# Kernel tuning notes

Measured on AMD Instinct MI355X. Metric: run time of the kernel, lower is better.

The kernel has to match this reference:

```python
import jax, jax.numpy as jnp
import numpy as np

PROCESSING_STEPS = 3


def setup_inputs() -> dict:
    key = jax.random.key(0)
    ks = jax.random.split(key, 6)
    N, D, G = 500000, 128, 4096
    x = jax.random.normal(ks[0], (N, D), dtype=jnp.float32)
    # torch LSTM param layout: [4*hidden, input] and [4*hidden, hidden], gates i,f,g,o
    s = 1.0 / np.sqrt(D)
    W_ih = jax.random.uniform(ks[1], (4 * D, 2 * D), minval=-s, maxval=s, dtype=jnp.float32)
    W_hh = jax.random.uniform(ks[2], (4 * D, D), minval=-s, maxval=s, dtype=jnp.float32)
    b_ih = jax.random.uniform(ks[3], (4 * D,), minval=-s, maxval=s, dtype=jnp.float32)
    b_hh = jax.random.uniform(ks[4], (4 * D,), minval=-s, maxval=s, dtype=jnp.float32)
    index = jnp.sort(jax.random.randint(ks[5], (N,), 0, G, dtype=jnp.int64))
    return {"x": x, "W_ih": W_ih, "W_hh": W_hh, "b_ih": b_ih, "b_hh": b_hh,
            "index": index, "dim_size": G}


def _lstm_cell(inp, h, c, W_ih, W_hh, b_ih, b_hh):
    gates = inp @ W_ih.T + h @ W_hh.T + (b_ih + b_hh)  # [G, 4D]
    i, f, g, o = jnp.split(gates, 4, axis=-1)
    c = jax.nn.sigmoid(f) * c + jax.nn.sigmoid(i) * jnp.tanh(g)
    h = jax.nn.sigmoid(o) * jnp.tanh(c)
    return h, c


def reference(x, W_ih, W_hh, b_ih, b_hh, index, dim_size):
    N, D = x.shape
    h = jnp.zeros((dim_size, D), dtype=x.dtype)
    c = jnp.zeros((dim_size, D), dtype=x.dtype)
    q_star = jnp.zeros((dim_size, 2 * D), dtype=x.dtype)
    for _ in range(PROCESSING_STEPS):
        h, c = _lstm_cell(q_star, h, c, W_ih, W_hh, b_ih, b_hh)
        q = h  # [G, D]
        e = jnp.sum(x * q[index], axis=-1)  # [N]
        # segment softmax (numerically stable)
        m = jax.ops.segment_max(e, index, num_segments=dim_size)
        m = jnp.where(jnp.isfinite(m), m, 0.0)  # guard empty segments
        ex = jnp.exp(e - m[index])
        s = jax.ops.segment_sum(ex, index, num_segments=dim_size)
        a = ex / jnp.maximum(s, 1e-16)[index]  # [N]
        r = jax.ops.segment_sum(a[:, None] * x, index, num_segments=dim_size)  # [G, D]
        q_star = jnp.concatenate([q, r], axis=-1)
    return q_star
```

## Files before the change

### kernel.cpp

```cpp
#include <hip/hip_runtime.h>
#include <math.h>

#define D 128

__device__ __forceinline__ float sigmoidf_(float x) { return 1.f / (1.f + __expf(-x)); }

__global__ void prep_kernel(const float* __restrict__ W_ih, const float* __restrict__ W_hh,
                            const float* __restrict__ b_ih, const float* __restrict__ b_hh,
                            const int* __restrict__ idx, int N, int G,
                            float* __restrict__ Wc, int* __restrict__ seg_off,
                            float* __restrict__ b_sum, float* __restrict__ h1,
                            float* __restrict__ c1) {
    int b = blockIdx.x, t = threadIdx.x;
    if (b < 256) {
        int i = b * 256 + t;
        int j = i >> 7, k = i & (D - 1);
        Wc[i] = W_ih[(size_t)j * (2 * D) + k] + W_hh[i];
    } else if (b < 273) {
        int g = (b - 256) * 256 + t;
        if (g <= G) {
            int lo = 0, hi = N;
            while (lo < hi) {
                int mid = (lo + hi) >> 1;
                if (idx[mid] < g) lo = mid + 1; else hi = mid;
            }
            seg_off[g] = lo;
        }
    } else {
        for (int i = t; i < 4 * D; i += 256) b_sum[i] = b_ih[i] + b_hh[i];
        if (t < D) {
            float bi = b_ih[t] + b_hh[t];
            float bg = b_ih[2 * D + t] + b_hh[2 * D + t];
            float bo = b_ih[3 * D + t] + b_hh[3 * D + t];
            float c = sigmoidf_(bi) * tanhf(bg);
            c1[t] = c;
            h1[t] = sigmoidf_(bo) * tanhf(c);
        }
    }
}

__global__ __launch_bounds__(256) void attn_kernel(
    const float* __restrict__ x, const int* __restrict__ seg_off,
    const float* __restrict__ q, int q_stride,
    float* __restrict__ r_out, int r_stride, int G) {
    int g = blockIdx.x;
    if (g >= G) return;
    int tid = threadIdx.x;
    int wave = tid >> 6, lane = tid & 63;
    int half = lane >> 5, col4 = lane & 31;

    __shared__ float sm[4], ss[4];
    __shared__ float sacc[4][D];

    int start = seg_off[g], end = seg_off[g + 1];
    int count = end - start;
    int chunk = (count + 3) >> 2;
    int wsr = start + wave * chunk;
    int wer = min(wsr + chunk, end);

    const float4* x4 = (const float4*)x;
    const float4* q4 = (const float4*)(q + (size_t)g * q_stride);
    float4 qv = q4[col4];

    float m = -INFINITY, s = 0.f;
    float4 acc = {0.f, 0.f, 0.f, 0.f};

    if (wsr < wer) {
        int last = wer - 1;
        int ngroups = (wer - wsr + 7) >> 3;
        for (int it = 0; it < ngroups; ++it) {
            int base = wsr + it * 8;
            int ra = min(base + 0 + half, last);
            int rb = min(base + 2 + half, last);
            int rc = min(base + 4 + half, last);
            int rd = min(base + 6 + half, last);
            float4 xa = x4[(size_t)ra * 32 + col4];
            float4 xb = x4[(size_t)rb * 32 + col4];
            float4 xc = x4[(size_t)rc * 32 + col4];
            float4 xd = x4[(size_t)rd * 32 + col4];

            float pa = xa.x * qv.x + xa.y * qv.y + xa.z * qv.z + xa.w * qv.w;
            float pb = xb.x * qv.x + xb.y * qv.y + xb.z * qv.z + xb.w * qv.w;
            float pc = xc.x * qv.x + xc.y * qv.y + xc.z * qv.z + xc.w * qv.w;
            float pd = xd.x * qv.x + xd.y * qv.y + xd.z * qv.z + xd.w * qv.w;
#pragma unroll
            for (int off = 1; off < 32; off <<= 1) {
                pa += __shfl_xor(pa, off);
                pb += __shfl_xor(pb, off);
                pc += __shfl_xor(pc, off);
                pd += __shfl_xor(pd, off);
            }
            float oa = __shfl_xor(pa, 32);
            float ob = __shfl_xor(pb, 32);
            float oc = __shfl_xor(pc, 32);
            float od = __shfl_xor(pd, 32);
            float pae = half ? oa : pa, pao = half ? pa : oa;
            float pbe = half ? ob : pb, pbo = half ? pb : ob;
            float pce = half ? oc : pc, pco = half ? pc : oc;
            float pde = half ? od : pd, pdo = half ? pd : od;
            pae = (base + 0 < wer) ? pae : -INFINITY;
            pao = (base + 1 < wer) ? pao : -INFINITY;
            pbe = (base + 2 < wer) ? pbe : -INFINITY;
            pbo = (base + 3 < wer) ? pbo : -INFINITY;
            pce = (base + 4 < wer) ? pce : -INFINITY;
            pco = (base + 5 < wer) ? pco : -INFINITY;
            pde = (base + 6 < wer) ? pde : -INFINITY;
            pdo = (base + 7 < wer) ? pdo : -INFINITY;

            float mn = fmaxf(fmaxf(fmaxf(pae, pao), fmaxf(pbe, pbo)),
                             fmaxf(fmaxf(pce, pco), fmaxf(pde, pdo)));
            mn = fmaxf(m, mn);
            float al = __expf(m - mn);
            float wae = __expf(pae - mn), wao = __expf(pao - mn);
            float wbe = __expf(pbe - mn), wbo = __expf(pbo - mn);
            float wce = __expf(pce - mn), wco = __expf(pco - mn);
            float wde = __expf(pde - mn), wdo = __expf(pdo - mn);
            float sg = (wae + wao) + (wbe + wbo) + ((wce + wco) + (wde + wdo));
            s = s * al + sg;
            float wsa = half ? wao : wae;
            float wsb = half ? wbo : wbe;
            float wsc = half ? wco : wce;
            float wsd = half ? wdo : wde;
            float tx = wsa * xa.x + wsb * xb.x + wsc * xc.x + wsd * xd.x;
            float ty = wsa * xa.y + wsb * xb.y + wsc * xc.y + wsd * xd.y;
            float tz = wsa * xa.z + wsb * xb.z + wsc * xc.z + wsd * xd.z;
            float tw = wsa * xa.w + wsb * xb.w + wsc * xc.w + wsd * xd.w;
            acc.x = acc.x * al + tx;
            acc.y = acc.y * al + ty;
            acc.z = acc.z * al + tz;
            acc.w = acc.w * al + tw;
            m = mn;
        }
    }
    acc.x += __shfl_xor(acc.x, 32);
    acc.y += __shfl_xor(acc.y, 32);
    acc.z += __shfl_xor(acc.z, 32);
    acc.w += __shfl_xor(acc.w, 32);

    if (lane == 0) { sm[wave] = m; ss[wave] = s; }
    if (half == 0) *(float4*)&sacc[wave][col4 * 4] = acc;
    __syncthreads();

    if (tid < D) {
        float m0 = sm[0], m1 = sm[1], m2 = sm[2], m3 = sm[3];
        float mstar = fmaxf(fmaxf(m0, m1), fmaxf(m2, m3));
        float r = 0.f;
        if (mstar > -INFINITY) {
            float e0 = __expf(m0 - mstar), e1 = __expf(m1 - mstar);
            float e2 = __expf(m2 - mstar), e3 = __expf(m3 - mstar);
            float stot = ss[0] * e0 + ss[1] * e1 + ss[2] * e2 + ss[3] * e3;
            float at = sacc[0][tid] * e0 + sacc[1][tid] * e1
                     + sacc[2][tid] * e2 + sacc[3][tid] * e3;
            r = at / fmaxf(stot, 1e-16f);
        }
        r_out[(size_t)g * r_stride + tid] = r;
    }
}

__global__ __launch_bounds__(256) void gates_gemm_kernel(
    const float* __restrict__ A1, int sA1,
    const float* __restrict__ W1,
    const float* __restrict__ A2,
    const float* __restrict__ W2, int sW2,
    const float* __restrict__ bias,
    float* __restrict__ gates) {
    __shared__ float As[32][72];
    __shared__ float Ws[32][72];
    int t = threadIdx.x;
    int tx = t & 15, ty = t >> 4;
    int g0 = blockIdx.x * 64, j0 = blockIdx.y * 64;
    int lr = t & 63;
    int lk = (t >> 6) * 8;

    float acc[4][4];
#pragma unroll
    for (int i = 0; i < 4; ++i)
#pragma unroll
        for (int j = 0; j < 4; ++j) acc[i][j] = 0.f;

    for (int phase = 0; phase < 2; ++phase) {
        const float* A = phase ? A2 : A1;
        int sA = phase ? D : sA1;
        const float* W = phase ? W2 : W1;
        int sW = phase ? sW2 : D;
        for (int kk = 0; kk < D; kk += 32) {
            float4 a0 = *(const float4*)&A[(size_t)(g0 + lr) * sA + kk + lk];
            float4 a1 = *(const float4*)&A[(size_t)(g0 + lr) * sA + kk + lk + 4];
            float4 w0 = *(const float4*)&W[(size_t)(j0 + lr) * sW + kk + lk];
            float4 w1 = *(const float4*)&W[(size_t)(j0 + lr) * sW + kk + lk + 4];
            __syncthreads();
            As[lk + 0][lr] = a0.x; As[lk + 1][lr] = a0.y; As[lk + 2][lr] = a0.z; As[lk + 3][lr] = a0.w;
            As[lk + 4][lr] = a1.x; As[lk + 5][lr] = a1.y; As[lk + 6][lr] = a1.z; As[lk + 7][lr] = a1.w;
            Ws[lk + 0][lr] = w0.x; Ws[lk + 1][lr] = w0.y; Ws[lk + 2][lr] = w0.z; Ws[lk + 3][lr] = w0.w;
            Ws[lk + 4][lr] = w1.x; Ws[lk + 5][lr] = w1.y; Ws[lk + 6][lr] = w1.z; Ws[lk + 7][lr] = w1.w;
            __syncthreads();
#pragma unroll
            for (int k = 0; k < 32; ++k) {
                float4 av = *(const float4*)&As[k][ty * 4];
                float4 bv = *(const float4*)&Ws[k][tx * 4];
                float aa[4] = {av.x, av.y, av.z, av.w};
                float bb[4] = {bv.x, bv.y, bv.z, bv.w};
#pragma unroll
                for (int i = 0; i < 4; ++i)
#pragma unroll
                    for (int j = 0; j < 4; ++j)
                        acc[i][j] = fmaf(aa[i], bb[j], acc[i][j]);
            }
        }
    }
#pragma unroll
    for (int i = 0; i < 4; ++i) {
        size_t row = (size_t)(g0 + ty * 4 + i);
        int jb = j0 + tx * 4;
        float4 o;
        o.x = acc[i][0] + bias[jb + 0];
        o.y = acc[i][1] + bias[jb + 1];
        o.z = acc[i][2] + bias[jb + 2];
        o.w = acc[i][3] + bias[jb + 3];
        *(float4*)&gates[row * 512 + jb] = o;
    }
}

__global__ void cell_kernel(const float* __restrict__ gates,
                            const float* __restrict__ c_prev, int c_stride,
                            float* __restrict__ c_out,
                            float* __restrict__ h_out, int h_stride,
                            int total) {
    int t = blockIdx.x * blockDim.x + threadIdx.x;
    if (t >= total) return;
    int g = t >> 7, k = t & (D - 1);
    const float* grow = gates + (size_t)g * 512;
    float ig = grow[k];
    float fg = grow[D + k];
    float gg = grow[2 * D + k];
    float og = grow[3 * D + k];
    float cp = c_prev[(size_t)g * c_stride + k];
    float c = sigmoidf_(fg) * cp + sigmoidf_(ig) * tanhf(gg);
    float h = sigmoidf_(og) * tanhf(c);
    c_out[t] = c;
    h_out[(size_t)g * h_stride + k] = h;
}

extern "C" void kernel_launch(void* const* d_in, const int* in_sizes, int n_in,
                              void* d_out, int out_size, void* d_ws, size_t ws_size,
                              hipStream_t stream) {
    const float* x      = (const float*)d_in[0];
    const float* W_ih   = (const float*)d_in[1];
    const float* W_hh   = (const float*)d_in[2];
    const float* b_ih   = (const float*)d_in[3];
    const float* b_hh   = (const float*)d_in[4];
    const int*   index  = (const int*)d_in[5];
    int N = in_sizes[5];
    int G = out_size / (2 * D);
    float* out = (float*)d_out;

    float* ws = (float*)d_ws;
    float* Wc     = ws;
    float* b_sum  = Wc + 4 * D * D;
    float* h1     = b_sum + 4 * D;
    float* c1     = h1 + D;
    float* r1     = c1 + D;
    float* h2     = r1 + (size_t)G * D;
    float* c2     = h2 + (size_t)G * D;
    float* r2     = c2 + (size_t)G * D;
    float* gatesb = r2 + (size_t)G * D;
    int* seg_off  = (int*)(gatesb + (size_t)G * 4 * D);
    float* c3     = r1;

    prep_kernel<<<274, 256, 0, stream>>>(W_ih, W_hh, b_ih, b_hh, index, N, G,
                                         Wc, seg_off, b_sum, h1, c1);

    attn_kernel<<<G, 256, 0, stream>>>(x, seg_off, h1, 0, r1, D, G);

    gates_gemm_kernel<<<dim3(G / 64, 8), 256, 0, stream>>>(
        h1, 0, Wc, r1, W_ih + D, 2 * D, b_sum, gatesb);
    cell_kernel<<<(G * D + 255) / 256, 256, 0, stream>>>(gatesb, c1, 0, c2, h2, D, G * D);
    attn_kernel<<<G, 256, 0, stream>>>(x, seg_off, h2, D, r2, D, G);

    gates_gemm_kernel<<<dim3(G / 64, 8), 256, 0, stream>>>(
        h2, D, Wc, r2, W_ih + D, 2 * D, b_sum, gatesb);
    cell_kernel<<<(G * D + 255) / 256, 256, 0, stream>>>(gatesb, c2, D, c3, out, 2 * D, G * D);
    attn_kernel<<<G, 256, 0, stream>>>(x, seg_off, out, 2 * D, out + D, 2 * D, G);
}
```

Baseline: 494.6 us.

## Double-buffer segment rows through LDS with register-staged prefetch in attention kernel

The attention kernel now walks each segment in tiles of 32 rows. The whole block cooperatively loads each tile into a double-buffered 32 KB shared-memory array, prefetching the next tile into registers while the current one is processed. This replaces the old scheme, where each wave owned a contiguous quarter of the segment and read rows straight from global memory. The goal is to overlap global loads with compute and to keep coalesced, fully occupied loads. In exchange it adds a __syncthreads per tile, uses 32 KB of LDS per block (which lowers occupancy), and does more masked work at tile tails.

```diff
diff --git a/kernel.cpp b/kernel.cpp
--- a/kernel.cpp
+++ b/kernel.cpp
@@ -42,21 +42,20 @@
 __global__ __launch_bounds__(256) void attn_kernel(
     const float* __restrict__ x, const int* __restrict__ seg_off,
     const float* __restrict__ q, int q_stride,
-    float* __restrict__ r_out, int r_stride, int G) {
+    float* __restrict__ r_out, int r_stride, int G, int N) {
     int g = blockIdx.x;
     if (g >= G) return;
     int tid = threadIdx.x;
     int wave = tid >> 6, lane = tid & 63;
     int half = lane >> 5, col4 = lane & 31;
 
+    __shared__ float xs[2][32 * D];
     __shared__ float sm[4], ss[4];
     __shared__ float sacc[4][D];
 
     int start = seg_off[g], end = seg_off[g + 1];
     int count = end - start;
-    int chunk = (count + 3) >> 2;
-    int wsr = start + wave * chunk;
-    int wer = min(wsr + chunk, end);
+    int T = (count + 31) >> 5;
 
     const float4* x4 = (const float4*)x;
     const float4* q4 = (const float4*)(q + (size_t)g * q_stride);
@@ -65,19 +64,45 @@
     float m = -INFINITY, s = 0.f;
     float4 acc = {0.f, 0.f, 0.f, 0.f};
 
-    if (wsr < wer) {
-        int last = wer - 1;
-        int ngroups = (wer - wsr + 7) >> 3;
-        for (int it = 0; it < ngroups; ++it) {
-            int base = wsr + it * 8;
-            int ra = min(base + 0 + half, last);
-            int rb = min(base + 2 + half, last);
-            int rc = min(base + 4 + half, last);
-            int rd = min(base + 6 + half, last);
-            float4 xa = x4[(size_t)ra * 32 + col4];
-            float4 xb = x4[(size_t)rb * 32 + col4];
-            float4 xc = x4[(size_t)rc * 32 + col4];
-            float4 xd = x4[(size_t)rd * 32 + col4];
+    size_t gmax = (size_t)N * 32 - 1;
+
+    if (T > 0) {
+        size_t b4 = (size_t)start * 32;
+        size_t i0 = b4 + tid, i1 = b4 + 256 + tid, i2 = b4 + 512 + tid, i3 = b4 + 768 + tid;
+        float4 v0 = x4[i0 < gmax ? i0 : gmax];
+        float4 v1 = x4[i1 < gmax ? i1 : gmax];
+        float4 v2 = x4[i2 < gmax ? i2 : gmax];
+        float4 v3 = x4[i3 < gmax ? i3 : gmax];
+        *(float4*)&xs[0][(tid) * 4]       = v0;
+        *(float4*)&xs[0][(256 + tid) * 4] = v1;
+        *(float4*)&xs[0][(512 + tid) * 4] = v2;
+        *(float4*)&xs[0][(768 + tid) * 4] = v3;
+    }
+
+    for (int t = 0; t < T; ++t) {
+        int cur = t & 1;
+        __syncthreads();
+
+        float4 st0, st1, st2, st3;
+        bool more = (t + 1 < T);
+        if (more) {
+            size_t b4 = (size_t)(start + (t + 1) * 32) * 32;
+            size_t i0 = b4 + tid, i1 = b4 + 256 + tid, i2 = b4 + 512 + tid, i3 = b4 + 768 + tid;
+            st0 = x4[i0 < gmax ? i0 : gmax];
+            st1 = x4[i1 < gmax ? i1 : gmax];
+            st2 = x4[i2 < gmax ? i2 : gmax];
+            st3 = x4[i3 < gmax ? i3 : gmax];
+        }
+
+        int tbase = t * 32 + wave * 8;
+        if (tbase < count) {
+            int vr = count - tbase;
+            const float* ls = &xs[cur][0];
+            int rb = wave * 8 + half;
+            float4 xa = *(const float4*)&ls[(rb + 0) * D + col4 * 4];
+            float4 xb = *(const float4*)&ls[(rb + 2) * D + col4 * 4];
+            float4 xc = *(const float4*)&ls[(rb + 4) * D + col4 * 4];
+            float4 xd = *(const float4*)&ls[(rb + 6) * D + col4 * 4];
 
             float pa = xa.x * qv.x + xa.y * qv.y + xa.z * qv.z + xa.w * qv.w;
             float pb = xb.x * qv.x + xb.y * qv.y + xb.z * qv.z + xb.w * qv.w;
@@ -98,14 +123,13 @@
             float pbe = half ? ob : pb, pbo = half ? pb : ob;
             float pce = half ? oc : pc, pco = half ? pc : oc;
             float pde = half ? od : pd, pdo = half ? pd : od;
-            pae = (base + 0 < wer) ? pae : -INFINITY;
-            pao = (base + 1 < wer) ? pao : -INFINITY;
-            pbe = (base + 2 < wer) ? pbe : -INFINITY;
-            pbo = (base + 3 < wer) ? pbo : -INFINITY;
-            pce = (base + 4 < wer) ? pce : -INFINITY;
-            pco = (base + 5 < wer) ? pco : -INFINITY;
-            pde = (base + 6 < wer) ? pde : -INFINITY;
-            pdo = (base + 7 < wer) ? pdo : -INFINITY;
+            pao = (1 < vr) ? pao : -INFINITY;
+            pbe = (2 < vr) ? pbe : -INFINITY;
+            pbo = (3 < vr) ? pbo : -INFINITY;
+            pce = (4 < vr) ? pce : -INFINITY;
+            pco = (5 < vr) ? pco : -INFINITY;
+            pde = (6 < vr) ? pde : -INFINITY;
+            pdo = (7 < vr) ? pdo : -INFINITY;
 
             float mn = fmaxf(fmaxf(fmaxf(pae, pao), fmaxf(pbe, pbo)),
                              fmaxf(fmaxf(pce, pco), fmaxf(pde, pdo)));
@@ -131,7 +155,16 @@
             acc.w = acc.w * al + tw;
             m = mn;
         }
-    }
+
+        if (more) {
+            float* ld = &xs[1 - cur][0];
+            *(float4*)&ld[(tid) * 4]       = st0;
+            *(float4*)&ld[(256 + tid) * 4] = st1;
+            *(float4*)&ld[(512 + tid) * 4] = st2;
+            *(float4*)&ld[(768 + tid) * 4] = st3;
+        }
+    }
+
     acc.x += __shfl_xor(acc.x, 32);
     acc.y += __shfl_xor(acc.y, 32);
     acc.z += __shfl_xor(acc.z, 32);
@@ -270,15 +303,15 @@
     prep_kernel<<<274, 256, 0, stream>>>(W_ih, W_hh, b_ih, b_hh, index, N, G,
                                          Wc, seg_off, b_sum, h1, c1);
 
-    attn_kernel<<<G, 256, 0, stream>>>(x, seg_off, h1, 0, r1, D, G);
+    attn_kernel<<<G, 256, 0, stream>>>(x, seg_off, h1, 0, r1, D, G, N);
 
     gates_gemm_kernel<<<dim3(G / 64, 8), 256, 0, stream>>>(
         h1, 0, Wc, r1, W_ih + D, 2 * D, b_sum, gatesb);
     cell_kernel<<<(G * D + 255) / 256, 256, 0, stream>>>(gatesb, c1, 0, c2, h2, D, G * D);
-    attn_kernel<<<G, 256, 0, stream>>>(x, seg_off, h2, D, r2, D, G);
+    attn_kernel<<<G, 256, 0, stream>>>(x, seg_off, h2, D, r2, D, G, N);
 
     gates_gemm_kernel<<<dim3(G / 64, 8), 256, 0, stream>>>(
         h2, D, Wc, r2, W_ih + D, 2 * D, b_sum, gatesb);
     cell_kernel<<<(G * D + 255) / 256, 256, 0, stream>>>(gatesb, c2, D, c3, out, 2 * D, G * D);
-    attn_kernel<<<G, 256, 0, stream>>>(x, seg_off, out, 2 * D, out + D, 2 * D, G);
-}
+    attn_kernel<<<G, 256, 0, stream>>>(x, seg_off, out, 2 * D, out + D, 2 * D, G, N);
+}
```

Measured after the change: 506.3 us. 1.02x slower.

## Convert x to fp16 once per call and read half-precision rows in attention

Applied to the files above, without the earlier changes.

Adds a kernel that converts x to fp16 into workspace once per call. All three attention passes then read half-size rows, with 16 lanes per row and 8 elements per lane, instead of 32 lanes of float4. This is meant to halve the bytes each attention pass streams, and the fp16 copy may fit in the large last-level cache. It adds one extra full read of x plus a write of the fp16 copy, and fp16 rounding of x may hurt accuracy.

```diff
diff --git a/kernel.cpp b/kernel.cpp
--- a/kernel.cpp
+++ b/kernel.cpp
@@ -1,4 +1,5 @@
 #include <hip/hip_runtime.h>
+#include <hip/hip_fp16.h>
 #include <math.h>
 
 #define D 128
@@ -39,15 +40,31 @@
     }
 }
 
+__global__ __launch_bounds__(256) void x_to_h_kernel(const float* __restrict__ x,
+                                                     __half* __restrict__ xh,
+                                                     size_t total) {
+    size_t i = ((size_t)blockIdx.x * 256 + threadIdx.x) * 8;
+    if (i >= total) return;
+    float4 a = *(const float4*)&x[i];
+    float4 b = *(const float4*)&x[i + 4];
+    __half2 h[4];
+    h[0] = __floats2half2_rn(a.x, a.y);
+    h[1] = __floats2half2_rn(a.z, a.w);
+    h[2] = __floats2half2_rn(b.x, b.y);
+    h[3] = __floats2half2_rn(b.z, b.w);
+    *(float4*)&xh[i] = *(float4*)h;
+}
+
 __global__ __launch_bounds__(256) void attn_kernel(
-    const float* __restrict__ x, const int* __restrict__ seg_off,
+    const __half* __restrict__ xh, const int* __restrict__ seg_off,
     const float* __restrict__ q, int q_stride,
     float* __restrict__ r_out, int r_stride, int G) {
     int g = blockIdx.x;
     if (g >= G) return;
     int tid = threadIdx.x;
     int wave = tid >> 6, lane = tid & 63;
-    int half = lane >> 5, col4 = lane & 31;
+    int qg = lane >> 4;
+    int c = lane & 15;
 
     __shared__ float sm[4], ss[4];
     __shared__ float sacc[4][D];
@@ -58,87 +75,76 @@
     int wsr = start + wave * chunk;
     int wer = min(wsr + chunk, end);
 
-    const float4* x4 = (const float4*)x;
-    const float4* q4 = (const float4*)(q + (size_t)g * q_stride);
-    float4 qv = q4[col4];
+    const float4* x4 = (const float4*)xh;
+    const float* qrow = q + (size_t)g * q_stride;
+    float4 q0 = *(const float4*)&qrow[8 * c];
+    float4 q1 = *(const float4*)&qrow[8 * c + 4];
 
     float m = -INFINITY, s = 0.f;
-    float4 acc = {0.f, 0.f, 0.f, 0.f};
+    float acc[8] = {0.f, 0.f, 0.f, 0.f, 0.f, 0.f, 0.f, 0.f};
 
     if (wsr < wer) {
         int last = wer - 1;
-        int ngroups = (wer - wsr + 7) >> 3;
-        for (int it = 0; it < ngroups; ++it) {
-            int base = wsr + it * 8;
-            int ra = min(base + 0 + half, last);
-            int rb = min(base + 2 + half, last);
-            int rc = min(base + 4 + half, last);
-            int rd = min(base + 6 + half, last);
-            float4 xa = x4[(size_t)ra * 32 + col4];
-            float4 xb = x4[(size_t)rb * 32 + col4];
-            float4 xc = x4[(size_t)rc * 32 + col4];
-            float4 xd = x4[(size_t)rd * 32 + col4];
-
-            float pa = xa.x * qv.x + xa.y * qv.y + xa.z * qv.z + xa.w * qv.w;
-            float pb = xb.x * qv.x + xb.y * qv.y + xb.z * qv.z + xb.w * qv.w;
-            float pc = xc.x * qv.x + xc.y * qv.y + xc.z * qv.z + xc.w * qv.w;
-            float pd = xd.x * qv.x + xd.y * qv.y + xd.z * qv.z + xd.w * qv.w;
-#pragma unroll
-            for (int off = 1; off < 32; off <<= 1) {
-                pa += __shfl_xor(pa, off);
-                pb += __shfl_xor(pb, off);
-                pc += __shfl_xor(pc, off);
-                pd += __shfl_xor(pd, off);
+        for (int base = wsr; base < wer; base += 8) {
+            int r0 = min(base + qg, last);
+            int r1 = min(base + 4 + qg, last);
+            float4 v0 = x4[(size_t)r0 * 16 + c];
+            float4 v1 = x4[(size_t)r1 * 16 + c];
+            const __half2* h0 = (const __half2*)&v0;
+            const __half2* h1 = (const __half2*)&v1;
+            float2 a0 = __half22float2(h0[0]), a1 = __half22float2(h0[1]);
+            float2 a2 = __half22float2(h0[2]), a3 = __half22float2(h0[3]);
+            float2 b0 = __half22float2(h1[0]), b1 = __half22float2(h1[1]);
+            float2 b2 = __half22float2(h1[2]), b3 = __half22float2(h1[3]);
+            float xf0[8] = {a0.x, a0.y, a1.x, a1.y, a2.x, a2.y, a3.x, a3.y};
+            float xf1[8] = {b0.x, b0.y, b1.x, b1.y, b2.x, b2.y, b3.x, b3.y};
+
+            float p0 = xf0[0] * q0.x + xf0[1] * q0.y + xf0[2] * q0.z + xf0[3] * q0.w
+                     + xf0[4] * q1.x + xf0[5] * q1.y + xf0[6] * q1.z + xf0[7] * q1.w;
+            float p1 = xf1[0] * q0.x + xf1[1] * q0.y + xf1[2] * q0.z + xf1[3] * q0.w
+                     + xf1[4] * q1.x + xf1[5] * q1.y + xf1[6] * q1.z + xf1[7] * q1.w;
+#pragma unroll
+            for (int off = 1; off < 16; off <<= 1) {
+                p0 += __shfl_xor(p0, off);
+                p1 += __shfl_xor(p1, off);
             }
-            float oa = __shfl_xor(pa, 32);
-            float ob = __shfl_xor(pb, 32);
-            float oc = __shfl_xor(pc, 32);
-            float od = __shfl_xor(pd, 32);
-            float pae = half ? oa : pa, pao = half ? pa : oa;
-            float pbe = half ? ob : pb, pbo = half ? pb : ob;
-            float pce = half ? oc : pc, pco = half ? pc : oc;
-            float pde = half ? od : pd, pdo = half ? pd : od;
-            pae = (base + 0 < wer) ? pae : -INFINITY;
-            pao = (base + 1 < wer) ? pao : -INFINITY;
-            pbe = (base + 2 < wer) ? pbe : -INFINITY;
-            pbo = (base + 3 < wer) ? pbo : -INFINITY;
-            pce = (base + 4 < wer) ? pce : -INFINITY;
-            pco = (base + 5 < wer) ? pco : -INFINITY;
-            pde = (base + 6 < wer) ? pde : -INFINITY;
-            pdo = (base + 7 < wer) ? pdo : -INFINITY;
-
-            float mn = fmaxf(fmaxf(fmaxf(pae, pao), fmaxf(pbe, pbo)),
-                             fmaxf(fmaxf(pce, pco), fmaxf(pde, pdo)));
+            float p0a = __shfl_xor(p0, 16), p0b = __shfl_xor(p0, 32), p0c = __shfl_xor(p0a, 32);
+            float p1a = __shfl_xor(p1, 16), p1b = __shfl_xor(p1, 32), p1c = __shfl_xor(p1a, 32);
+            float s00 = (base + qg       < wer) ? p0  : -INFINITY;
+            float s01 = (base + (qg ^ 1) < wer) ? p0a : -INFINITY;
+            float s02 = (base + (qg ^ 2) < wer) ? p0b : -INFINITY;
+            float s03 = (base + (qg ^ 3) < wer) ? p0c : -INFINITY;
+            float s10 = (base + 4 + qg       < wer) ? p1  : -INFINITY;
+            float s11 = (base + 4 + (qg ^ 1) < wer) ? p1a : -INFINITY;
+            float s12 = (base + 4 + (qg ^ 2) < wer) ? p1b : -INFINITY;
+            float s13 = (base + 4 + (qg ^ 3) < wer) ? p1c : -INFINITY;
+
+            float mn = fmaxf(fmaxf(fmaxf(s00, s01), fmaxf(s02, s03)),
+                             fmaxf(fmaxf(s10, s11), fmaxf(s12, s13)));
             mn = fmaxf(m, mn);
             float al = __expf(m - mn);
-            float wae = __expf(pae - mn), wao = __expf(pao - mn);
-            float wbe = __expf(pbe - mn), wbo = __expf(pbo - mn);
-            float wce = __expf(pce - mn), wco = __expf(pco - mn);
-            float wde = __expf(pde - mn), wdo = __expf(pdo - mn);
-            float sg = (wae + wao) + (wbe + wbo) + ((wce + wco) + (wde + wdo));
+            float w00 = __expf(s00 - mn), w01 = __expf(s01 - mn);
+            float w02 = __expf(s02 - mn), w03 = __expf(s03 - mn);
+            float w10 = __expf(s10 - mn), w11 = __expf(s11 - mn);
+            float w12 = __expf(s12 - mn), w13 = __expf(s13 - mn);
+            float sg = (w00 + w01) + (w02 + w03) + ((w10 + w11) + (w12 + w13));
             s = s * al + sg;
-            float wsa = half ? wao : wae;
-            float wsb = half ? wbo : wbe;
-            float wsc = half ? wco : wce;
-            float wsd = half ? wdo : wde;
-            float tx = wsa * xa.x + wsb * xb.x + wsc * xc.x + wsd * xd.x;
-            float ty = wsa * xa.y + wsb * xb.y + wsc * xc.y + wsd * xd.y;
-            float tz = wsa * xa.z + wsb * xb.z + wsc * xc.z + wsd * xd.z;
-            float tw = wsa * xa.w + wsb * xb.w + wsc * xc.w + wsd * xd.w;
-            acc.x = acc.x * al + tx;
-            acc.y = acc.y * al + ty;
-            acc.z = acc.z * al + tz;
-            acc.w = acc.w * al + tw;
+#pragma unroll
+            for (int j = 0; j < 8; ++j)
+                acc[j] = acc[j] * al + w00 * xf0[j] + w10 * xf1[j];
             m = mn;
         }
     }
-    acc.x += __shfl_xor(acc.x, 32);
-    acc.y += __shfl_xor(acc.y, 32);
-    acc.z += __shfl_xor(acc.z, 32);
-    acc.w += __shfl_xor(acc.w, 32);
-
+#pragma unroll
+    for (int j = 0; j < 8; ++j) {
+        acc[j] += __shfl_xor(acc[j], 16);
+        acc[j] += __shfl_xor(acc[j], 32);
+    }
     if (lane == 0) { sm[wave] = m; ss[wave] = s; }
-    if (half == 0) *(float4*)&sacc[wave][col4 * 4] = acc;
+    if (qg == 0) {
+#pragma unroll
+        for (int j = 0; j < 8; ++j) sacc[wave][8 * c + j] = acc[j];
+    }
     __syncthreads();
 
     if (tid < D) {
@@ -253,9 +259,11 @@
     int N = in_sizes[5];
     int G = out_size / (2 * D);
     float* out = (float*)d_out;
+    size_t totalx = (size_t)N * D;
 
     float* ws = (float*)d_ws;
-    float* Wc     = ws;
+    __half* xh    = (__half*)ws;
+    float* Wc     = ws + totalx / 2;
     float* b_sum  = Wc + 4 * D * D;
     float* h1     = b_sum + 4 * D;
     float* c1     = h1 + D;
@@ -269,16 +277,17 @@
 
     prep_kernel<<<274, 256, 0, stream>>>(W_ih, W_hh, b_ih, b_hh, index, N, G,
                                          Wc, seg_off, b_sum, h1, c1);
-
-    attn_kernel<<<G, 256, 0, stream>>>(x, seg_off, h1, 0, r1, D, G);
+    x_to_h_kernel<<<(int)((totalx / 8 + 255) / 256), 256, 0, stream>>>(x, xh, totalx);
+
+    attn_kernel<<<G, 256, 0, stream>>>(xh, seg_off, h1, 0, r1, D, G);
 
     gates_gemm_kernel<<<dim3(G / 64, 8), 256, 0, stream>>>(
         h1, 0, Wc, r1, W_ih + D, 2 * D, b_sum, gatesb);
     cell_kernel<<<(G * D + 255) / 256, 256, 0, stream>>>(gatesb, c1, 0, c2, h2, D, G * D);
-    attn_kernel<<<G, 256, 0, stream>>>(x, seg_off, h2, D, r2, D, G);
+    attn_kernel<<<G, 256, 0, stream>>>(xh, seg_off, h2, D, r2, D, G);
 
     gates_gemm_kernel<<<dim3(G / 64, 8), 256, 0, stream>>>(
         h2, D, Wc, r2, W_ih + D, 2 * D, b_sum, gatesb);
     cell_kernel<<<(G * D + 255) / 256, 256, 0, stream>>>(gatesb, c2, D, c3, out, 2 * D, G * D);
-    attn_kernel<<<G, 256, 0, stream>>>(x, seg_off, out, 2 * D, out + D, 2 * D, G);
-}
+    attn_kernel<<<G, 256, 0, stream>>>(xh, seg_off, out, 2 * D, out + D, 2 * D, G);
+}
```

Result: no change. 492.3 us (-0.5%).
